# Optimization experiments

Measured on AMD Instinct MI355X. Metric: run time of the kernel, lower is better.

Reference implementation:

```python
import jax, jax.numpy as jnp
import numpy as np

B, M, H = 1024, 32, 2
D = 64
N_ENT = 500000
N_REL = 32


def setup_inputs() -> dict:
    key = jax.random.key(0)
    k1, k2, k3, k4 = jax.random.split(key, 4)
    edge_index = jax.random.randint(k1, (B, 2), 0, N_ENT, dtype=jnp.int64)
    # column 0: head entity ids, column 1: relation ids; keep both < N_REL so both are in-range
    ripple_sets = jax.random.randint(k2, (H, B, M, 2), 0, N_REL, dtype=jnp.int64)
    entity_emb = jax.random.normal(k3, (N_ENT, D), dtype=jnp.float32)
    relation_emb = jax.random.normal(k4, (N_REL, D * D), dtype=jnp.float32)
    # padding_idx=0 -> row 0 is zeros
    entity_emb = entity_emb.at[0].set(0.0)
    relation_emb = relation_emb.at[0].set(0.0)
    return {
        "edge_index": edge_index,
        "ripple_sets": ripple_sets,
        "entity_emb": entity_emb,
        "relation_emb": relation_emb,
    }


def reference(edge_index, ripple_sets, entity_emb, relation_emb):
    d = entity_emb.shape[1]
    item = entity_emb[edge_index[:, 1]]            # [B, d]
    u = jnp.zeros_like(item)                       # [B, d]
    for hop in range(ripple_sets.shape[0]):        # small fixed hop count
        rs = ripple_sets[hop]                      # [B, M, 2]
        R = relation_emb[rs[:, :, 1]].reshape(rs.shape[0], -1, d, d)  # [B, M, d, d]
        h = entity_emb[rs[:, :, 0]]                # [B, M, d]
        Rh = jnp.einsum('bmij,bmj->bmi', R, h)     # [B, M, d]
        vRh = jnp.einsum('bmi,bi->bm', Rh, item)   # [B, M]
        p = jax.nn.softmax(vRh, axis=1)            # [B, M]
        u = u + jnp.einsum('bm,bmd->bd', p, h)     # weighted sum of tails (t == h)
    return jnp.sum(u * item, axis=1, keepdims=True)  # [B, 1]
```

## Files before the change

### kernel.cpp

```cpp
#include <hip/hip_runtime.h>
#include <math.h>

#define BB   1024
#define MM   32
#define HH   2
#define DD   64
#define NREL 32
#define TBB  32

__global__ __launch_bounds__(256) void compute_q(
    const int* __restrict__ edge_index,
    const float* __restrict__ entity_emb,
    const float* __restrict__ relation_emb,
    float* __restrict__ qout)
{
    __shared__ float R_s[DD * DD];
    __shared__ float item_s[TBB * 68];

    const int r   = blockIdx.y;
    const int b0  = blockIdx.x * TBB;
    const int tid = threadIdx.x;

    const float4* Rg = (const float4*)(relation_emb + (size_t)r * DD * DD);
    #pragma unroll
    for (int k = 0; k < 4; ++k)
        ((float4*)R_s)[tid + 256 * k] = Rg[tid + 256 * k];

    #pragma unroll
    for (int k = 0; k < 2; ++k) {
        int idx = tid + 256 * k;
        int bl  = idx >> 4;
        int c4  = idx & 15;
        int ei  = edge_index[2 * (b0 + bl) + 1];
        ((float4*)(item_s + bl * 68))[c4] =
            *(const float4*)(entity_emb + (size_t)ei * DD + c4 * 4);
    }
    __syncthreads();

    const int j4  = (tid & 15) * 4;
    const int bl0 = tid >> 4;
    float4 acc0 = {0.f, 0.f, 0.f, 0.f};
    float4 acc1 = {0.f, 0.f, 0.f, 0.f};
    #pragma unroll 8
    for (int i = 0; i < DD; ++i) {
        const float4 rv = *(const float4*)(R_s + i * DD + j4);
        const float a0 = item_s[bl0 * 68 + i];
        const float a1 = item_s[(bl0 + 16) * 68 + i];
        acc0.x += a0 * rv.x; acc0.y += a0 * rv.y;
        acc0.z += a0 * rv.z; acc0.w += a0 * rv.w;
        acc1.x += a1 * rv.x; acc1.y += a1 * rv.y;
        acc1.z += a1 * rv.z; acc1.w += a1 * rv.w;
    }
    size_t q0 = ((size_t)(b0 + bl0) * NREL + r) * DD + j4;
    size_t q1 = ((size_t)(b0 + bl0 + 16) * NREL + r) * DD + j4;
    *(float4*)(qout + q0) = acc0;
    *(float4*)(qout + q1) = acc1;
}

#define HS 65

__global__ __launch_bounds__(256) void ripple_apply(
    const int* __restrict__ edge_index,
    const int* __restrict__ ripple_sets,
    const float* __restrict__ entity_emb,
    const float* __restrict__ qg,
    float* __restrict__ out)
{
    __shared__ float item_s[DD];
    __shared__ float h_s[HH * MM * HS];
    __shared__ float q_s[HH * MM * HS];
    __shared__ float vp_s[4 * 64];
    __shared__ float p_s[HH * MM];
    __shared__ float up_s[4 * 68];

    const int b   = blockIdx.x;
    const int tid = threadIdx.x;

    if (tid < DD) {
        int item_idx = edge_index[2 * b + 1];
        item_s[tid] = entity_emb[(size_t)item_idx * DD + tid];
    }

    #pragma unroll
    for (int k = 0; k < 4; ++k) {
        int idx = tid + 256 * k;
        int row = idx >> 4;
        int c4  = idx & 15;
        int hop = row >> 5, m = row & 31;
        size_t ibase = ((size_t)(hop * BB + b) * MM + m) * 2;
        int head = ripple_sets[ibase];
        int rel  = ripple_sets[ibase + 1];
        const float4 hv = *(const float4*)(entity_emb + (size_t)head * DD + c4 * 4);
        float* hd = h_s + row * HS + c4 * 4;
        hd[0] = hv.x; hd[1] = hv.y; hd[2] = hv.z; hd[3] = hv.w;
        const float4 qv = *(const float4*)(qg + ((size_t)b * NREL + rel) * DD + c4 * 4);
        float* qd = q_s + row * HS + c4 * 4;
        qd[0] = qv.x; qd[1] = qv.y; qd[2] = qv.z; qd[3] = qv.w;
    }
    __syncthreads();

    {
        int t = tid & 63;
        int q = tid >> 6;
        const float* qp = q_s + t * HS + q * 16;
        const float* hp = h_s + t * HS + q * 16;
        float acc = 0.f;
        #pragma unroll
        for (int j = 0; j < 16; ++j) acc += qp[j] * hp[j];
        vp_s[q * 64 + t] = acc;
    }
    __syncthreads();

    if (tid < HH * MM) {
        float v = vp_s[tid] + vp_s[64 + tid] + vp_s[128 + tid] + vp_s[192 + tid];
        float mx = v;
        #pragma unroll
        for (int off = 16; off > 0; off >>= 1)
            mx = fmaxf(mx, __shfl_xor(mx, off, 64));
        float e = expf(v - mx);
        float s = e;
        #pragma unroll
        for (int off = 16; off > 0; off >>= 1)
            s += __shfl_xor(s, off, 64);
        p_s[tid] = e / s;
    }
    __syncthreads();

    {
        int d    = tid & 63;
        int part = tid >> 6;
        float u = 0.f;
        #pragma unroll
        for (int tt = 0; tt < 16; ++tt) {
            int t = part * 16 + tt;
            u += p_s[t] * h_s[t * HS + d];
        }
        up_s[part * 68 + d] = u;
    }
    __syncthreads();

    if (tid < DD) {
        float u = up_s[tid] + up_s[68 + tid] + up_s[136 + tid] + up_s[204 + tid];
        float prod = u * item_s[tid];
        #pragma unroll
        for (int off = 32; off > 0; off >>= 1) prod += __shfl_down(prod, off, 64);
        if (tid == 0) out[b] = prod;
    }
}

extern "C" void kernel_launch(void* const* d_in, const int* in_sizes, int n_in,
                              void* d_out, int out_size, void* d_ws, size_t ws_size,
                              hipStream_t stream) {
    const int*   edge_index   = (const int*)d_in[0];
    const int*   ripple_sets  = (const int*)d_in[1];
    const float* entity_emb   = (const float*)d_in[2];
    const float* relation_emb = (const float*)d_in[3];
    float* out = (float*)d_out;
    float* qbuf = (float*)d_ws;
    (void)in_sizes; (void)n_in; (void)out_size; (void)ws_size;

    compute_q<<<dim3(BB / TBB, NREL), dim3(256), 0, stream>>>(
        edge_index, entity_emb, relation_emb, qbuf);
    ripple_apply<<<dim3(BB), dim3(256), 0, stream>>>(
        edge_index, ripple_sets, entity_emb, qbuf, out);
}
```

Measured before the change: 170.8 us.

## Fold item dot into per-row scalars and drop shared staging of h and q

Rewrites the per-sample kernel to use the identity sum(u*item) = sum_m p_m * (h_m·item), so each ripple row is reduced to two scalars (q·h and h·item) with wavefront shuffles right after loading. This removes the large shared-memory h/q tiles, the weighted-sum pass over h, and several barriers. It also loads head/relation ids as a single int2. Summation order changes slightly, which alters floating-point rounding.

```diff
diff --git a/kernel.cpp b/kernel.cpp
--- a/kernel.cpp
+++ b/kernel.cpp
@@ -57,8 +57,6 @@
     *(float4*)(qout + q1) = acc1;
 }
 
-#define HS 65
-
 __global__ __launch_bounds__(256) void ripple_apply(
     const int* __restrict__ edge_index,
     const int* __restrict__ ripple_sets,
@@ -66,53 +64,39 @@
     const float* __restrict__ qg,
     float* __restrict__ out)
 {
-    __shared__ float item_s[DD];
-    __shared__ float h_s[HH * MM * HS];
-    __shared__ float q_s[HH * MM * HS];
-    __shared__ float vp_s[4 * 64];
-    __shared__ float p_s[HH * MM];
-    __shared__ float up_s[4 * 68];
+    __shared__ float v_s[HH * MM];
+    __shared__ float w_s[HH * MM];
 
     const int b   = blockIdx.x;
     const int tid = threadIdx.x;
+    const int c4  = tid & 15;
 
-    if (tid < DD) {
-        int item_idx = edge_index[2 * b + 1];
-        item_s[tid] = entity_emb[(size_t)item_idx * DD + tid];
-    }
+    const int item_idx = edge_index[2 * b + 1];
+    const float4 iv = *(const float4*)(entity_emb + (size_t)item_idx * DD + c4 * 4);
 
     #pragma unroll
     for (int k = 0; k < 4; ++k) {
         int idx = tid + 256 * k;
         int row = idx >> 4;
-        int c4  = idx & 15;
         int hop = row >> 5, m = row & 31;
-        size_t ibase = ((size_t)(hop * BB + b) * MM + m) * 2;
-        int head = ripple_sets[ibase];
-        int rel  = ripple_sets[ibase + 1];
-        const float4 hv = *(const float4*)(entity_emb + (size_t)head * DD + c4 * 4);
-        float* hd = h_s + row * HS + c4 * 4;
-        hd[0] = hv.x; hd[1] = hv.y; hd[2] = hv.z; hd[3] = hv.w;
-        const float4 qv = *(const float4*)(qg + ((size_t)b * NREL + rel) * DD + c4 * 4);
-        float* qd = q_s + row * HS + c4 * 4;
-        qd[0] = qv.x; qd[1] = qv.y; qd[2] = qv.z; qd[3] = qv.w;
-    }
-    __syncthreads();
-
-    {
-        int t = tid & 63;
-        int q = tid >> 6;
-        const float* qp = q_s + t * HS + q * 16;
-        const float* hp = h_s + t * HS + q * 16;
-        float acc = 0.f;
+        size_t ibase = (size_t)(hop * BB + b) * MM + m;
+        const int2 hr = ((const int2*)ripple_sets)[ibase];
+        const float4 hv = *(const float4*)(entity_emb + (size_t)hr.x * DD + c4 * 4);
+        const float4 qv = *(const float4*)(qg + ((size_t)b * NREL + hr.y) * DD + c4 * 4);
+        float sv = hv.x * qv.x + hv.y * qv.y + hv.z * qv.z + hv.w * qv.w;
+        float sw = hv.x * iv.x + hv.y * iv.y + hv.z * iv.z + hv.w * iv.w;
         #pragma unroll
-        for (int j = 0; j < 16; ++j) acc += qp[j] * hp[j];
-        vp_s[q * 64 + t] = acc;
+        for (int off = 8; off > 0; off >>= 1) {
+            sv += __shfl_xor(sv, off, 64);
+            sw += __shfl_xor(sw, off, 64);
+        }
+        if (c4 == 0) { v_s[row] = sv; w_s[row] = sw; }
     }
     __syncthreads();
 
     if (tid < HH * MM) {
-        float v = vp_s[tid] + vp_s[64 + tid] + vp_s[128 + tid] + vp_s[192 + tid];
+        float v = v_s[tid];
+        float w = w_s[tid];
         float mx = v;
         #pragma unroll
         for (int off = 16; off > 0; off >>= 1)
@@ -122,29 +106,11 @@
         #pragma unroll
         for (int off = 16; off > 0; off >>= 1)
             s += __shfl_xor(s, off, 64);
-        p_s[tid] = e / s;
-    }
-    __syncthreads();
-
-    {
-        int d    = tid & 63;
-        int part = tid >> 6;
-        float u = 0.f;
+        float contrib = (e / s) * w;
         #pragma unroll
-        for (int tt = 0; tt < 16; ++tt) {
-            int t = part * 16 + tt;
-            u += p_s[t] * h_s[t * HS + d];
-        }
-        up_s[part * 68 + d] = u;
-    }
-    __syncthreads();
-
-    if (tid < DD) {
-        float u = up_s[tid] + up_s[68 + tid] + up_s[136 + tid] + up_s[204 + tid];
-        float prod = u * item_s[tid];
-        #pragma unroll
-        for (int off = 32; off > 0; off >>= 1) prod += __shfl_down(prod, off, 64);
-        if (tid == 0) out[b] = prod;
+        for (int off = 32; off > 0; off >>= 1)
+            contrib += __shfl_xor(contrib, off, 64);
+        if (tid == 0) out[b] = contrib;
     }
 }
 
```

Result: no change. 172.6 us (+1.1%).
